# Optimization experiments

Measured on AMD Instinct MI355X. Metric: run time of the kernel, lower is better.

Reference implementation:

```python
import jax, jax.numpy as jnp
import numpy as np

N_NODES = 100000
N_EDGES = 3200000


def _spmm(edge_row, edge_col, edge_val, h):
    # out[i] = sum_{e: row[e]==i} val[e] * h[col[e]]
    msgs = edge_val[:, None] * h[edge_col]  # [E, F]
    return jax.ops.segment_sum(msgs, edge_row, num_segments=N_NODES)


def _gc_layer(x, W, b, edge_row, edge_col, edge_val):
    # GraphConvolution: support = x @ W; out = spmm(adj, support) + b
    support = x @ W
    return _spmm(edge_row, edge_col, edge_val, support) + b


def setup_inputs() -> dict:
    key = jax.random.key(0)
    ks = jax.random.split(key, 8)
    F_IN, HID, C = 512, 256, 40
    x = jax.random.normal(ks[0], (N_NODES, F_IN), dtype=jnp.float32)
    W1 = jax.random.normal(ks[1], (F_IN, HID), dtype=jnp.float32) * (1.0 / np.sqrt(F_IN))
    b1 = jnp.zeros((HID,), dtype=jnp.float32)
    W2 = jax.random.normal(ks[2], (HID, C), dtype=jnp.float32) * (1.0 / np.sqrt(HID))
    b2 = jnp.zeros((C,), dtype=jnp.float32)
    edge_row = jax.random.randint(ks[3], (N_EDGES,), 0, N_NODES, dtype=jnp.int32)
    edge_col = jax.random.randint(ks[4], (N_EDGES,), 0, N_NODES, dtype=jnp.int32)
    edge_val = jax.random.uniform(ks[5], (N_EDGES,), dtype=jnp.float32) * 0.05
    return {"x": x, "W1": W1, "b1": b1, "W2": W2, "b2": b2,
            "edge_row": edge_row, "edge_col": edge_col, "edge_val": edge_val}


def reference(x, W1, b1, W2, b2, edge_row, edge_col, edge_val):
    h = jax.nn.relu(_gc_layer(x, W1, b1, edge_row, edge_col, edge_val))
    # dropout: inference mode (training=False) -> identity
    logits = _gc_layer(h, W2, b2, edge_row, edge_col, edge_val)
    return (jax.nn.log_softmax(logits, axis=1), jax.nn.softmax(logits, axis=1))
```

## Files before the change

### kernel.cpp

```cpp
#include <hip/hip_runtime.h>
#include <hip/hip_bf16.h>

#define N_NODES 100000
#define N_EDGES 3200000
#define F_IN    512
#define HID     256
#define C_OUT   40

#define RPB     512
#define BSHIFT  9
#define NBUCK   196
#define CAP     20480
#define GSTR    16

typedef unsigned short u16;
typedef unsigned char  u8;
typedef __attribute__((ext_vector_type(4))) unsigned short u16x4;
typedef __attribute__((ext_vector_type(8))) short bf16x8;
typedef __attribute__((ext_vector_type(4))) float f32x4;
typedef __attribute__((ext_vector_type(2))) float f32x2;

__device__ __forceinline__ float bf2f(u16 u) {
    unsigned int x = ((unsigned int)u) << 16;
    return __uint_as_float(x);
}
__device__ __forceinline__ u16 f2bf(float f) {
    unsigned int x = __float_as_uint(f);
    return (u16)((x + 0x7fffu + ((x >> 16) & 1u)) >> 16);
}
__device__ __forceinline__ unsigned int pk2(float lo, float hi) {
    return (unsigned int)f2bf(lo) | ((unsigned int)f2bf(hi) << 16);
}
__device__ __forceinline__ u8 f2fp8(float f) {
    return (u8)(__builtin_amdgcn_cvt_pk_fp8_f32(f, f, 0u, false) & 0xFF);
}


__global__ __launch_bounds__(1024) void k_p1(const int* __restrict__ row,
                                             const int* __restrict__ col,
                                             const float* __restrict__ val,
                                             int* __restrict__ gfill,
                                             int2* __restrict__ bpack) {
    __shared__ int hist[NBUCK];
    __shared__ int base[NBUCK];
    int t = threadIdx.x;
    for (int j = t; j < NBUCK; j += 1024) hist[j] = 0;
    __syncthreads();
    int e0 = blockIdx.x * 4096;
    int bin[4], key[4], lr[4];
    float vl[4];
#pragma unroll
    for (int u = 0; u < 4; u++) {
        int i = e0 + u * 1024 + t;
        if (i < N_EDGES) {
            int r = row[i];
            bin[u] = r >> BSHIFT;
            key[u] = (col[i] << BSHIFT) | (r & (RPB - 1));
            vl[u] = val[i];
            lr[u] = atomicAdd(&hist[bin[u]], 1);
        } else {
            bin[u] = -1;
        }
    }
    __syncthreads();
    for (int j = t; j < NBUCK; j += 1024)
        base[j] = atomicAdd(&gfill[j * GSTR], hist[j]);
    __syncthreads();
#pragma unroll
    for (int u = 0; u < 4; u++) {
        if (bin[u] >= 0) {
            int p = base[bin[u]] + lr[u];
            if (p < CAP)
                bpack[(size_t)bin[u] * CAP + p] = make_int2(key[u], __float_as_int(vl[u]));
        }
    }
}

__global__ void k_bscan(const int* __restrict__ gfill,
                        int* __restrict__ bucket_base,
                        int* __restrict__ row_off) {
    if (threadIdx.x == 0 && blockIdx.x == 0) {
        int run = 0;
        for (int b = 0; b < NBUCK; b++) {
            bucket_base[b] = run;
            run += gfill[b * GSTR];
        }
        row_off[N_NODES] = run;
    }
}

__global__ __launch_bounds__(1024) void k_p2(const int2* __restrict__ bpack,
                                             const int* __restrict__ gfill,
                                             const int* __restrict__ bucket_base,
                                             int2* __restrict__ cpack,
                                             int* __restrict__ row_off) {
    __shared__ int cnt[RPB];
    __shared__ int sc[RPB];
    __shared__ int rbase[RPB];
    int b = blockIdx.x, t = threadIdx.x;
    int n = gfill[b * GSTR];
    if (n > CAP) n = CAP;
    int gbase = bucket_base[b];
    if (t < RPB) cnt[t] = 0;
    __syncthreads();
    int key[20], lr[20];
    float v[20];
#pragma unroll
    for (int u = 0; u < 20; u++) {
        int i = u * 1024 + t;
        if (i < n) {
            int2 p = bpack[(size_t)b * CAP + i];
            key[u] = p.x;
            v[u] = __int_as_float(p.y);
            lr[u] = atomicAdd(&cnt[key[u] & (RPB - 1)], 1);
        } else {
            key[u] = -1;
        }
    }
    __syncthreads();
    if (t < RPB) sc[t] = cnt[t];
    __syncthreads();
    for (int off = 1; off < RPB; off <<= 1) {
        int x = 0;
        if (t < RPB && t >= off) x = sc[t - off];
        __syncthreads();
        if (t < RPB) sc[t] += x;
        __syncthreads();
    }
    if (t < RPB) rbase[t] = (t == 0) ? 0 : sc[t - 1];
    __syncthreads();
    int g0 = b * RPB;
    if (t < RPB && (g0 + t) < N_NODES) row_off[g0 + t] = gbase + rbase[t];
#pragma unroll
    for (int u = 0; u < 20; u++) {
        if (key[u] >= 0) {
            int pos = gbase + rbase[key[u] & (RPB - 1)] + lr[u];
            cpack[pos] = make_int2(key[u] >> BSHIFT, __float_as_int(v[u]));
        }
    }
}


__global__ __launch_bounds__(256) void k_cvtW1(const float* __restrict__ W1,
                                               u16* __restrict__ W1t) {
    int i = blockIdx.x * 256 + threadIdx.x;
    int k = i >> 8, n = i & 255;
    W1t[(size_t)n * F_IN + k] = f2bf(W1[i]);
}

__global__ __launch_bounds__(256) void k_cvtW2(const float* __restrict__ W2,
                                               u16* __restrict__ W2t) {
    int i = blockIdx.x * 256 + threadIdx.x;
    int n = i >> 8, k = i & 255;
    W2t[i] = (n < C_OUT) ? f2bf(W2[k * C_OUT + n]) : (u16)0;
}


#define ASTR 40
#define BSTR 40

__global__ __launch_bounds__(512) void k_gemm1(const float* __restrict__ A,
                                               const u16* __restrict__ Bt,
                                               u8* __restrict__ Cf8, int M) {
    __shared__ u16 As[2][128 * ASTR];
    __shared__ u16 Bs[2][256 * BSTR];
    int tid = threadIdx.x;
    int bm = blockIdx.x * 128;
    int lane = tid & 63, wid = tid >> 6;
    int wm = wid >> 2, wn = wid & 3;

    int s_ar = tid >> 2;
    int s_ak = (tid & 3) * 8;
    int s_bn = tid >> 1;
    int s_bk = (tid & 1) * 16;

    bool arow_ok = (bm + s_ar) < M;
    const float* aptr = A + (size_t)(bm + s_ar) * F_IN + s_ak;
    const u16*   bptr = Bt + (size_t)s_bn * F_IN + s_bk;

    f32x4 acc[4][4];
#pragma unroll
    for (int i = 0; i < 4; i++)
#pragma unroll
        for (int j = 0; j < 4; j++) acc[i][j] = (f32x4){0.f, 0.f, 0.f, 0.f};

    float4 ra0, ra1;
    int4 rb0, rb1;

    auto LOAD = [&](int kt) {
        const float* ap = aptr + kt * 32;
        if (arow_ok) {
            ra0 = *(const float4*)ap;
            ra1 = *(const float4*)(ap + 4);
        } else {
            ra0 = make_float4(0.f, 0.f, 0.f, 0.f);
            ra1 = ra0;
        }
        const u16* bp = bptr + kt * 32;
        rb0 = *(const int4*)bp;
        rb1 = *(const int4*)(bp + 8);
    };
    auto WRITE = [&](int buf) {
        int4 w;
        w.x = pk2(ra0.x, ra0.y);
        w.y = pk2(ra0.z, ra0.w);
        w.z = pk2(ra1.x, ra1.y);
        w.w = pk2(ra1.z, ra1.w);
        *(int4*)&As[buf][s_ar * ASTR + s_ak] = w;
        *(int4*)&Bs[buf][s_bn * BSTR + s_bk] = rb0;
        *(int4*)&Bs[buf][s_bn * BSTR + s_bk + 8] = rb1;
    };

    int kg = lane >> 4;
    int r16 = lane & 15;

    auto COMPUTE = [&](int buf) {
        bf16x8 a[4], b[4];
#pragma unroll
        for (int mt = 0; mt < 4; mt++)
            a[mt] = *(const bf16x8*)&As[buf][(wm * 64 + mt * 16 + r16) * ASTR + kg * 8];
#pragma unroll
        for (int nt = 0; nt < 4; nt++)
            b[nt] = *(const bf16x8*)&Bs[buf][(wn * 64 + nt * 16 + r16) * BSTR + kg * 8];
#pragma unroll
        for (int mt = 0; mt < 4; mt++)
#pragma unroll
            for (int nt = 0; nt < 4; nt++)
                acc[mt][nt] = __builtin_amdgcn_mfma_f32_16x16x32_bf16(
                    a[mt], b[nt], acc[mt][nt], 0, 0, 0);
    };

    LOAD(0);
    WRITE(0);
    __syncthreads();
#pragma unroll 1
    for (int kt = 0; kt < F_IN / 32; kt++) {
        int cur = kt & 1;
        if (kt < F_IN / 32 - 1) LOAD(kt + 1);
        COMPUTE(cur);
        if (kt < F_IN / 32 - 1) WRITE(cur ^ 1);
        __syncthreads();
    }

#pragma unroll
    for (int mt = 0; mt < 4; mt++) {
        int r0 = bm + wm * 64 + mt * 16 + (lane >> 4) * 4;
#pragma unroll
        for (int nt = 0; nt < 4; nt++) {
            int c = wn * 64 + nt * 16 + (lane & 15);
#pragma unroll
            for (int j = 0; j < 4; j++) {
                int r = r0 + j;
                if (r < M) Cf8[(size_t)r * HID + c] = f2fp8(acc[mt][nt][j]);
            }
        }
    }
}


__global__ __launch_bounds__(256) void k_spmm1(const u8* __restrict__ Sf8,
                                               const int2* __restrict__ cpack,
                                               const int* __restrict__ row_off,
                                               const float* __restrict__ b1,
                                               u16* __restrict__ Hb) {
    int lane = threadIdx.x & 63;
    int row = blockIdx.x * 4 + (threadIdx.x >> 6);
    int beg = __builtin_amdgcn_readfirstlane(row_off[row]);
    int end = __builtin_amdgcn_readfirstlane(row_off[row + 1]);
    int f4 = lane * 4;
    const u8* base = Sf8 + f4;
    float acc[4] = {};
    int e = beg;
    for (; e + 8 <= end; e += 8) {
        int2 q[8];
#pragma unroll
        for (int t = 0; t < 8; t++) q[t] = cpack[e + t];
#pragma unroll
        for (int t = 0; t < 8; t++) {
            float vv = __int_as_float(q[t].y);
            unsigned int w = *(const unsigned int*)(base + (size_t)q[t].x * HID);
            f32x2 lo = __builtin_amdgcn_cvt_pk_f32_fp8(w, false);
            f32x2 hi = __builtin_amdgcn_cvt_pk_f32_fp8(w, true);
            acc[0] += vv * lo.x;
            acc[1] += vv * lo.y;
            acc[2] += vv * hi.x;
            acc[3] += vv * hi.y;
        }
    }
    for (; e < end; e++) {
        int2 q = cpack[e];
        float vv = __int_as_float(q.y);
        unsigned int w = *(const unsigned int*)(base + (size_t)q.x * HID);
        f32x2 lo = __builtin_amdgcn_cvt_pk_f32_fp8(w, false);
        f32x2 hi = __builtin_amdgcn_cvt_pk_f32_fp8(w, true);
        acc[0] += vv * lo.x;
        acc[1] += vv * lo.y;
        acc[2] += vv * hi.x;
        acc[3] += vv * hi.y;
    }
    float4 b = *(const float4*)&b1[f4];
    u16x4 o;
    o.x = f2bf(fmaxf(acc[0] + b.x, 0.f));
    o.y = f2bf(fmaxf(acc[1] + b.y, 0.f));
    o.z = f2bf(fmaxf(acc[2] + b.z, 0.f));
    o.w = f2bf(fmaxf(acc[3] + b.w, 0.f));
    *(u16x4*)&Hb[(size_t)row * HID + f4] = o;
}


#define G2STR 264

__global__ __launch_bounds__(256) void k_gemm2(const u16* __restrict__ Hb,
                                               const u16* __restrict__ W2t,
                                               u8* __restrict__ S2f8) {
    __shared__ u16 As[64 * G2STR];
    int tid = threadIdx.x;
    int base = blockIdx.x * 64;
    {
        int r = tid >> 2, c0 = (tid & 3) * 64;
        const u16* src = Hb + (size_t)(base + r) * HID + c0;
        bool ok = (base + r) < N_NODES;
#pragma unroll
        for (int q = 0; q < 8; q++) {
            int4 d = ok ? *(const int4*)(src + q * 8) : make_int4(0, 0, 0, 0);
            *(int4*)&As[r * G2STR + c0 + q * 8] = d;
        }
    }
    __syncthreads();
    int lane = tid & 63, wv = tid >> 6;
    int r16 = lane & 15, kg = lane >> 4;
    f32x4 acc[4];
#pragma unroll
    for (int nt = 0; nt < 4; nt++) acc[nt] = (f32x4){0.f, 0.f, 0.f, 0.f};
#pragma unroll
    for (int ks = 0; ks < 8; ks++) {
        bf16x8 a = *(const bf16x8*)&As[(wv * 16 + r16) * G2STR + ks * 32 + kg * 8];
#pragma unroll
        for (int nt = 0; nt < 4; nt++) {
            bf16x8 b = *(const bf16x8*)&W2t[(size_t)(nt * 16 + r16) * 256 + ks * 32 + kg * 8];
            acc[nt] = __builtin_amdgcn_mfma_f32_16x16x32_bf16(a, b, acc[nt], 0, 0, 0);
        }
    }
    int orow = base + wv * 16 + (lane >> 4) * 4;
#pragma unroll
    for (int nt = 0; nt < 4; nt++) {
        int c = nt * 16 + r16;
        if (c < C_OUT) {
#pragma unroll
            for (int j = 0; j < 4; j++) {
                int r = orow + j;
                if (r < N_NODES) S2f8[(size_t)r * C_OUT + c] = f2fp8(acc[nt][j]);
            }
        }
    }
}


__global__ __launch_bounds__(256) void k_spmm2(const u8* __restrict__ S2f8,
                                               const int2* __restrict__ cpack,
                                               const int* __restrict__ row_off,
                                               const float* __restrict__ b2,
                                               float* __restrict__ out_ls,
                                               float* __restrict__ out_sm) {
    int lane = threadIdx.x & 63;
    int row = blockIdx.x * 4 + (threadIdx.x >> 6);
    int beg = __builtin_amdgcn_readfirstlane(row_off[row]);
    int end = __builtin_amdgcn_readfirstlane(row_off[row + 1]);
    int l = (lane < C_OUT) ? lane : 0;
    float acc = 0.f;
    int e = beg;
    for (; e + 8 <= end; e += 8) {
        int2 q[8];
#pragma unroll
        for (int t = 0; t < 8; t++) q[t] = cpack[e + t];
#pragma unroll
        for (int t = 0; t < 8; t++) {
            float vv = __int_as_float(q[t].y);
            unsigned int sv = S2f8[(size_t)q[t].x * C_OUT + l];
            acc += vv * __builtin_amdgcn_cvt_f32_fp8(sv, 0);
        }
    }
    for (; e < end; e++) {
        int2 q = cpack[e];
        unsigned int sv = S2f8[(size_t)q.x * C_OUT + l];
        acc += __int_as_float(q.y) * __builtin_amdgcn_cvt_f32_fp8(sv, 0);
    }
    float v = (lane < C_OUT) ? (acc + b2[l]) : -1e30f;
    float mx = v;
    for (int s = 32; s; s >>= 1) mx = fmaxf(mx, __shfl_xor(mx, s));
    float e2 = (lane < C_OUT) ? __expf(v - mx) : 0.f;
    float sum = e2;
    for (int s = 32; s; s >>= 1) sum += __shfl_xor(sum, s);
    float ls = v - mx - __logf(sum);
    float sm = e2 / sum;
    if (lane < C_OUT) {
        out_ls[(size_t)row * C_OUT + lane] = ls;
        out_sm[(size_t)row * C_OUT + lane] = sm;
    }
}


extern "C" void kernel_launch(void* const* d_in, const int* in_sizes, int n_in,
                              void* d_out, int out_size, void* d_ws, size_t ws_size,
                              hipStream_t stream) {
    const float* x    = (const float*)d_in[0];
    const float* W1   = (const float*)d_in[1];
    const float* b1   = (const float*)d_in[2];
    const float* W2   = (const float*)d_in[3];
    const float* b2   = (const float*)d_in[4];
    const int*   erow = (const int*)d_in[5];
    const int*   ecol = (const int*)d_in[6];
    const float* eval = (const float*)d_in[7];
    float* out = (float*)d_out;

    char* w = (char*)d_ws;
    auto alloc = [&](size_t bytes) {
        char* p = w;
        w += (bytes + 255) & ~(size_t)255;
        return p;
    };
    u8*    support = (u8*)   alloc((size_t)N_NODES * HID);
    u16*   hbuf    = (u16*)  alloc((size_t)N_NODES * HID * sizeof(u16));
    int2*  cpack   = (int2*) alloc((size_t)N_EDGES * sizeof(int2));
    int2*  bpack   = (int2*) alloc((size_t)NBUCK * CAP * sizeof(int2));
    int*   row_off = (int*)  alloc((size_t)(N_NODES + 1) * sizeof(int));
    int*   gfill   = (int*)  alloc((size_t)NBUCK * GSTR * sizeof(int));
    int*   bucket_base = (int*) alloc((size_t)NBUCK * sizeof(int));
    u8*    S2f8    = (u8*)   alloc((size_t)N_NODES * C_OUT);
    u16*   W2t     = (u16*)  alloc((size_t)64 * 256 * sizeof(u16));
    u16*   W1t     = (u16*)  alloc((size_t)F_IN * HID * sizeof(u16));

    hipMemsetAsync(gfill, 0, (size_t)NBUCK * GSTR * sizeof(int), stream);

    int NB1 = (N_EDGES + 4095) / 4096;
    k_p1<<<NB1, 1024, 0, stream>>>(erow, ecol, eval, gfill, bpack);
    k_bscan<<<1, 64, 0, stream>>>(gfill, bucket_base, row_off);
    k_p2<<<NBUCK, 1024, 0, stream>>>(bpack, gfill, bucket_base, cpack, row_off);

    k_cvtW1<<<(F_IN * HID) / 256, 256, 0, stream>>>(W1, W1t);
    k_cvtW2<<<(64 * 256) / 256, 256, 0, stream>>>(W2, W2t);
    k_gemm1<<<(N_NODES + 127) / 128, 512, 0, stream>>>(x, W1t, support, N_NODES);
    k_spmm1<<<N_NODES / 4, 256, 0, stream>>>(support, cpack, row_off, b1, hbuf);
    k_gemm2<<<(N_NODES + 63) / 64, 256, 0, stream>>>(hbuf, W2t, S2f8);
    k_spmm2<<<N_NODES / 4, 256, 0, stream>>>(S2f8, cpack, row_off, b2,
                                             out, out + (size_t)N_NODES * C_OUT);
}
```

Before: 381.2 us.

## Process six edges per wave in spmm2 with packed fp8 loads; unroll spmm1 by 16

In the second SpMM, each wave now splits into 6 groups of 10 lanes. Each lane loads 4 packed fp8 classes, so one wave iteration covers six edges instead of one, and partial sums are reduced through shared memory before the softmax. This cuts the number of serial edge iterations and uses wider loads. The first SpMM also gets a 16-edge unrolled loop ahead of the 8-edge loop to keep more gathers in flight. The shared-memory reduction relies on s_waitcnt rather than a barrier within the wave, which is a possible ordering risk.

```diff
diff --git a/kernel.cpp b/kernel.cpp
--- a/kernel.cpp
+++ b/kernel.cpp
@@ -271,6 +271,22 @@
     const u8* base = Sf8 + f4;
     float acc[4] = {};
     int e = beg;
+    for (; e + 16 <= end; e += 16) {
+        int2 q[16];
+#pragma unroll
+        for (int t = 0; t < 16; t++) q[t] = cpack[e + t];
+#pragma unroll
+        for (int t = 0; t < 16; t++) {
+            float vv = __int_as_float(q[t].y);
+            unsigned int w = *(const unsigned int*)(base + (size_t)q[t].x * HID);
+            f32x2 lo = __builtin_amdgcn_cvt_pk_f32_fp8(w, false);
+            f32x2 hi = __builtin_amdgcn_cvt_pk_f32_fp8(w, true);
+            acc[0] += vv * lo.x;
+            acc[1] += vv * lo.y;
+            acc[2] += vv * hi.x;
+            acc[3] += vv * hi.y;
+        }
+    }
     for (; e + 8 <= end; e += 8) {
         int2 q[8];
 #pragma unroll
@@ -362,30 +378,42 @@
                                                const float* __restrict__ b2,
                                                float* __restrict__ out_ls,
                                                float* __restrict__ out_sm) {
-    int lane = threadIdx.x & 63;
-    int row = blockIdx.x * 4 + (threadIdx.x >> 6);
+    __shared__ float red[4][64][4];
+    int tid = threadIdx.x;
+    int lane = tid & 63, wv = tid >> 6;
+    int row = blockIdx.x * 4 + wv;
     int beg = __builtin_amdgcn_readfirstlane(row_off[row]);
     int end = __builtin_amdgcn_readfirstlane(row_off[row + 1]);
-    int l = (lane < C_OUT) ? lane : 0;
-    float acc = 0.f;
-    int e = beg;
-    for (; e + 8 <= end; e += 8) {
-        int2 q[8];
-#pragma unroll
-        for (int t = 0; t < 8; t++) q[t] = cpack[e + t];
-#pragma unroll
-        for (int t = 0; t < 8; t++) {
-            float vv = __int_as_float(q[t].y);
-            unsigned int sv = S2f8[(size_t)q[t].x * C_OUT + l];
-            acc += vv * __builtin_amdgcn_cvt_f32_fp8(sv, 0);
-        }
-    }
-    for (; e < end; e++) {
-        int2 q = cpack[e];
-        unsigned int sv = S2f8[(size_t)q.x * C_OUT + l];
-        acc += __int_as_float(q.y) * __builtin_amdgcn_cvt_f32_fp8(sv, 0);
-    }
-    float v = (lane < C_OUT) ? (acc + b2[l]) : -1e30f;
+    int g = lane / 10;
+    int cb = (lane % 10) * 4;
+    bool act = lane < 60;
+    float acc[4] = {};
+    for (int e0 = beg; e0 < end; e0 += 6) {
+        int ei = e0 + g;
+        bool ok = act && (ei < end);
+        int2 q = cpack[ok ? ei : beg];
+        float vv = ok ? __int_as_float(q.y) : 0.f;
+        unsigned int w = *(const unsigned int*)(S2f8 + (size_t)q.x * C_OUT + cb);
+        f32x2 lo = __builtin_amdgcn_cvt_pk_f32_fp8(w, false);
+        f32x2 hi = __builtin_amdgcn_cvt_pk_f32_fp8(w, true);
+        acc[0] += vv * lo.x;
+        acc[1] += vv * lo.y;
+        acc[2] += vv * hi.x;
+        acc[3] += vv * hi.y;
+    }
+#pragma unroll
+    for (int j = 0; j < 4; j++) red[wv][lane][j] = acc[j];
+    __builtin_amdgcn_s_waitcnt(0);
+    float v;
+    if (lane < C_OUT) {
+        int sl = lane >> 2, j = lane & 3;
+        float s = 0.f;
+#pragma unroll
+        for (int gg = 0; gg < 6; gg++) s += red[wv][gg * 10 + sl][j];
+        v = s + b2[lane];
+    } else {
+        v = -1e30f;
+    }
     float mx = v;
     for (int s = 32; s; s >>= 1) mx = fmaxf(mx, __shfl_xor(mx, s));
     float e2 = (lane < C_OUT) ? __expf(v - mx) : 0.f;
```

New measurement: 382.4 us. About the same (+0.3%).
